# Kernel tuning notes

Hardware: AMD Instinct MI355X
Metric: run time of the kernel (lower is better)

## Reference

```python
import jax, jax.numpy as jnp
import numpy as np
from jax.ops import segment_sum

N_NODES = 100000


def _gcn_layer(x, W, b, src, dst, n_nodes):
    # DGL GraphConv with norm='both': out = D_in^{-1/2} A D_out^{-1/2} x W + b
    # degrees clamped to min 1 (DGL behavior, handles zero-degree nodes)
    ones_e = jnp.ones(src.shape[0], dtype=x.dtype)
    deg_out = jnp.clip(segment_sum(ones_e, src, num_segments=n_nodes), 1.0)
    deg_in = jnp.clip(segment_sum(ones_e, dst, num_segments=n_nodes), 1.0)
    h = x * jax.lax.rsqrt(deg_out)[:, None]            # [N, F] source norm
    agg = segment_sum(h[src], dst, num_segments=n_nodes)  # [N, F] sum over in-edges
    agg = agg * jax.lax.rsqrt(deg_in)[:, None]          # dest norm
    return agg @ W + b


def setup_inputs() -> dict:
    key = jax.random.key(0)
    k1, k2, k3, k4, k5 = jax.random.split(key, 5)
    E = 1600000
    x = jax.random.normal(k1, (N_NODES, 128), dtype=jnp.float32)
    edge_src = jax.random.randint(k2, (E,), 0, N_NODES, dtype=jnp.int32)
    edge_dst = jax.random.randint(k3, (E,), 0, N_NODES, dtype=jnp.int32)
    W1 = jax.random.normal(k4, (128, 64), dtype=jnp.float32) * (1.0 / np.sqrt(128))
    b1 = jnp.zeros((64,), dtype=jnp.float32)
    W2 = jax.random.normal(k5, (64, 64), dtype=jnp.float32) * (1.0 / np.sqrt(64))
    b2 = jnp.zeros((64,), dtype=jnp.float32)
    return {"x": x, "edge_src": edge_src, "edge_dst": edge_dst,
            "W1": W1, "b1": b1, "W2": W2, "b2": b2}


def reference(x, edge_src, edge_dst, W1, b1, W2, b2):
    h = _gcn_layer(x, W1, b1, edge_src, edge_dst, N_NODES)
    h = jax.nn.relu(h)
    out = _gcn_layer(h, W2, b2, edge_src, edge_dst, N_NODES)
    return out
```

## Files before the change

### kernel.cpp

```cpp
#include <hip/hip_runtime.h>
#include <hip/hip_fp16.h>


static inline size_t align256(size_t x) { return (x + 255) & ~(size_t)255; }

#define BKT_SHIFT 7
#define BKT_W 128
#define MAX_NBK 800
#define PA_BLOCKS 416

typedef _Float16 f16x8 __attribute__((ext_vector_type(8)));
typedef float f32x4 __attribute__((ext_vector_type(4)));

__global__ __launch_bounds__(256)
void part_hist_kernel(const int* __restrict__ src, const int* __restrict__ dst,
                      int* __restrict__ hist_d, int* __restrict__ hist_s,
                      int nbk, int E, int slice_len) {
    __shared__ int hd[MAX_NBK];
    __shared__ int hs[MAX_NBK];
    const int b = blockIdx.x;
    for (int i = threadIdx.x; i < nbk; i += 256) { hd[i] = 0; hs[i] = 0; }
    __syncthreads();
    const int beg = b * slice_len;
    const int end = min(beg + slice_len, E);
    for (int i = beg + threadIdx.x; i < end; i += 256) {
        atomicAdd(&hd[dst[i] >> BKT_SHIFT], 1);
        atomicAdd(&hs[src[i] >> BKT_SHIFT], 1);
    }
    __syncthreads();
    for (int i = threadIdx.x; i < nbk; i += 256) {
        hist_d[(size_t)i * PA_BLOCKS + b] = hd[i];
        hist_s[(size_t)i * PA_BLOCKS + b] = hs[i];
    }
}

__global__ __launch_bounds__(512)
void row_scan_kernel(int* __restrict__ hist_d, int* __restrict__ hist_s,
                     int* __restrict__ Td, int* __restrict__ Ts, int nbk) {
    __shared__ int tmp[512];
    int j = blockIdx.x;
    int* row;
    int* T;
    if (j < nbk) { row = hist_d + (size_t)j * PA_BLOCKS; T = Td; }
    else         { j -= nbk; row = hist_s + (size_t)j * PA_BLOCKS; T = Ts; }
    const int t = threadIdx.x;
    int v = (t < PA_BLOCKS) ? row[t] : 0;
    tmp[t] = v;
    __syncthreads();
    for (int off = 1; off < 512; off <<= 1) {
        int u = (t >= off) ? tmp[t - off] : 0;
        __syncthreads();
        tmp[t] += u;
        __syncthreads();
    }
    if (t < PA_BLOCKS) row[t] = tmp[t] - v;
    if (t == 511) T[j] = tmp[511];
}

__global__ __launch_bounds__(1024)
void tot_scan_kernel(int* __restrict__ Td, int* __restrict__ Ts, int nbk) {
    __shared__ int tmp[1024];
    const int t = threadIdx.x;
    int v = (t < nbk) ? Td[t] : 0;
    tmp[t] = v;
    __syncthreads();
    for (int off = 1; off < 1024; off <<= 1) {
        int u = (t >= off) ? tmp[t - off] : 0;
        __syncthreads();
        tmp[t] += u;
        __syncthreads();
    }
    if (t < nbk) Td[t] = tmp[t] - v;
    __syncthreads();
    int v2 = (t < nbk) ? Ts[t] : 0;
    tmp[t] = v2;
    __syncthreads();
    for (int off = 1; off < 1024; off <<= 1) {
        int u = (t >= off) ? tmp[t - off] : 0;
        __syncthreads();
        tmp[t] += u;
        __syncthreads();
    }
    if (t < nbk) Ts[t] = tmp[t] - v2;
}

__global__ __launch_bounds__(256)
void part_scatter_kernel(const int* __restrict__ src, const int* __restrict__ dst,
                         const int* __restrict__ hist_d, const int* __restrict__ hist_s,
                         const int* __restrict__ Td, const int* __restrict__ Ts,
                         int* __restrict__ ebuf, unsigned char* __restrict__ sbuf,
                         int nbk, int E, int slice_len) {
    __shared__ int cur_d[MAX_NBK];
    __shared__ int cur_s[MAX_NBK];
    const int b = blockIdx.x;
    for (int i = threadIdx.x; i < nbk; i += 256) {
        cur_d[i] = Td[i] + hist_d[(size_t)i * PA_BLOCKS + b];
        cur_s[i] = Ts[i] + hist_s[(size_t)i * PA_BLOCKS + b];
    }
    __syncthreads();
    const int beg = b * slice_len;
    const int end = min(beg + slice_len, E);
    for (int i = beg + threadIdx.x; i < end; i += 256) {
        int d = dst[i], s = src[i];
        int pd = atomicAdd(&cur_d[d >> BKT_SHIFT], 1);
        ebuf[pd] = ((d & (BKT_W - 1)) << 17) | s;
        int ps = atomicAdd(&cur_s[s >> BKT_SHIFT], 1);
        sbuf[ps] = (unsigned char)(s & (BKT_W - 1));
    }
}

__global__ __launch_bounds__(256)
void bucket_csr_kernel(const int* __restrict__ ebuf,
                       const unsigned char* __restrict__ sbuf,
                       const int* __restrict__ Td, const int* __restrict__ Ts,
                       int* __restrict__ csr_src,
                       int* __restrict__ cnt_in, int* __restrict__ cnt_out,
                       int* __restrict__ row_ptr,
                       int nbk, int N, int E) {
    __shared__ int cnt[BKT_W];
    __shared__ int rp[BKT_W];
    __shared__ int cur[BKT_W];
    __shared__ int cnts[BKT_W];
    const int k = blockIdx.x;
    const int lo = k << BKT_SHIFT;
    const int span = min(BKT_W, N - lo);
    const int db = Td[k], de = (k + 1 < nbk) ? Td[k + 1] : E;
    const int sb = Ts[k], se = (k + 1 < nbk) ? Ts[k + 1] : E;
    const int t = threadIdx.x;

    if (t < BKT_W) { cnt[t] = 0; cnts[t] = 0; }
    __syncthreads();
    for (int i = db + t; i < de; i += 256) atomicAdd(&cnt[ebuf[i] >> 17], 1);
    for (int i = sb + t; i < se; i += 256) atomicAdd(&cnts[sbuf[i]], 1);
    __syncthreads();
    if (t < BKT_W) rp[t] = cnt[t];
    __syncthreads();
    for (int off = 1; off < BKT_W; off <<= 1) {
        int v = (t < BKT_W && t >= off) ? rp[t - off] : 0;
        __syncthreads();
        if (t < BKT_W) rp[t] += v;
        __syncthreads();
    }
    if (t < span) {
        row_ptr[lo + t] = db + rp[t] - cnt[t];
        cnt_in[lo + t]  = cnt[t];
        cnt_out[lo + t] = cnts[t];
    }
    __syncthreads();
    if (t < BKT_W) cur[t] = db + rp[t] - cnt[t];
    __syncthreads();
    for (int i = db + t; i < de; i += 256) {
        int p = ebuf[i];
        int pos = atomicAdd(&cur[p >> 17], 1);
        csr_src[pos] = p & 0x1FFFF;
    }
    if (k == 0 && t == 0) row_ptr[N] = E;
}

template <int K>
__global__ __launch_bounds__(256)
void gemm_scale_kernel(const float* __restrict__ X, const float* __restrict__ W,
                       const int* __restrict__ cnt_out,
                       __half* __restrict__ Y, int N) {
    __shared__ _Float16 Wt[2][64][K + 8];
    const int t = threadIdx.x;
    for (int i = t; i < K * 64; i += 256) {
        const int k = i >> 6, j = i & 63;
        const float w = W[i];
        const _Float16 hi = (_Float16)w;
        Wt[0][j][k] = hi;
        Wt[1][j][k] = (_Float16)(w - (float)hi);
    }
    __syncthreads();

    const int wid  = t >> 6;
    const int lane = t & 63;
    const int col  = lane & 15;
    const int kg   = (lane >> 4) * 8;

    const int rowA = blockIdx.x * 64 + wid * 16 + col;
    const size_t xbase = (size_t)min(rowA, N - 1) * K;

    f32x4 acc0 = {}, acc1 = {}, acc2 = {}, acc3 = {};

#pragma unroll
    for (int ks = 0; ks < K; ks += 32) {
        float4 xa = *(const float4*)&X[xbase + ks + kg];
        float4 xb = *(const float4*)&X[xbase + ks + kg + 4];
        const float xs[8] = {xa.x, xa.y, xa.z, xa.w, xb.x, xb.y, xb.z, xb.w};
        f16x8 ahi, alo;
#pragma unroll
        for (int j = 0; j < 8; ++j) {
            const _Float16 h = (_Float16)xs[j];
            ahi[j] = h;
            alo[j] = (_Float16)(xs[j] - (float)h);
        }
#pragma unroll
        for (int tile = 0; tile < 4; ++tile) {
            const f16x8 bhi = *(const f16x8*)&Wt[0][col + 16 * tile][ks + kg];
            const f16x8 blo = *(const f16x8*)&Wt[1][col + 16 * tile][ks + kg];
            f32x4* acc = (tile == 0) ? &acc0 : (tile == 1) ? &acc1
                       : (tile == 2) ? &acc2 : &acc3;
            *acc = __builtin_amdgcn_mfma_f32_16x16x32_f16(ahi, bhi, *acc, 0, 0, 0);
            *acc = __builtin_amdgcn_mfma_f32_16x16x32_f16(alo, bhi, *acc, 0, 0, 0);
            *acc = __builtin_amdgcn_mfma_f32_16x16x32_f16(ahi, blo, *acc, 0, 0, 0);
        }
    }

    const int rbase = blockIdx.x * 64 + wid * 16 + (lane >> 4) * 4;
#pragma unroll
    for (int r = 0; r < 4; ++r) {
        const int rr = rbase + r;
        if (rr < N) {
            const float sc = rsqrtf((float)max(cnt_out[rr], 1));
            __half* yp = &Y[(size_t)rr * 64 + col];
            yp[0]  = __float2half_rn(acc0[r] * sc);
            yp[16] = __float2half_rn(acc1[r] * sc);
            yp[32] = __float2half_rn(acc2[r] * sc);
            yp[48] = __float2half_rn(acc3[r] * sc);
        }
    }
}

template <bool RELU>
__global__ __launch_bounds__(256)
void aggregate_kernel(const __half* __restrict__ Y,
                      const int* __restrict__ row_ptr,
                      const int* __restrict__ csr_src,
                      const int* __restrict__ cnt_in,
                      const float* __restrict__ bias,
                      float* __restrict__ out, int N) {
    const int n = blockIdx.x * 8 + (threadIdx.x >> 5);
    if (n >= N) return;
    const int fp = threadIdx.x & 31;

    const int start = row_ptr[n];
    const int end   = row_ptr[n + 1];
    const int last  = end - 1;

    float2 acc = {0.f, 0.f};
    for (int e = start; e < end; e += 16) {
        int idx[16];
#pragma unroll
        for (int j = 0; j < 16; ++j) idx[j] = csr_src[min(e + j, last)];
        float2 v[16];
#pragma unroll
        for (int j = 0; j < 16; ++j)
            v[j] = __half22float2(*((const __half2*)(Y + ((size_t)idx[j] << 6)) + fp));
#pragma unroll
        for (int j = 0; j < 16; ++j)
            if (e + j < end) { acc.x += v[j].x; acc.y += v[j].y; }
    }

    const float sc = rsqrtf((float)max(cnt_in[n], 1));
    float2 o;
    o.x = acc.x * sc + bias[2 * fp];
    o.y = acc.y * sc + bias[2 * fp + 1];
    if (RELU) { o.x = fmaxf(o.x, 0.f); o.y = fmaxf(o.y, 0.f); }
    *(float2*)&out[((size_t)n << 6) + 2 * fp] = o;
}

extern "C" void kernel_launch(void* const* d_in, const int* in_sizes, int n_in,
                              void* d_out, int out_size, void* d_ws, size_t ws_size,
                              hipStream_t stream) {
    const float* x   = (const float*)d_in[0];
    const int*   src = (const int*)d_in[1];
    const int*   dst = (const int*)d_in[2];
    const float* W1  = (const float*)d_in[3];
    const float* b1  = (const float*)d_in[4];
    const float* W2  = (const float*)d_in[5];
    const float* b2  = (const float*)d_in[6];
    float* out = (float*)d_out;

    const int N = in_sizes[0] / 128;
    const int E = in_sizes[1];

    const int nbk = (N + BKT_W - 1) >> BKT_SHIFT;
    const int M = nbk * PA_BLOCKS;

    char* ws = (char*)d_ws;
    size_t off = 0;
    __half* Y       = (__half*)(ws + off); off = align256(off + (size_t)N * 64 * sizeof(__half));
    int* csr_src    = (int*)(ws + off);    off = align256(off + (size_t)E * sizeof(int));
    int* ebuf       = (int*)(ws + off);    off = align256(off + (size_t)E * sizeof(int));
    unsigned char* sbuf = (unsigned char*)(ws + off); off = align256(off + (size_t)E);
    int* hist_d     = (int*)(ws + off);    off = align256(off + (size_t)M * sizeof(int));
    int* hist_s     = (int*)(ws + off);    off = align256(off + (size_t)M * sizeof(int));
    int* Td         = (int*)(ws + off);    off = align256(off + (size_t)nbk * sizeof(int));
    int* Ts         = (int*)(ws + off);    off = align256(off + (size_t)nbk * sizeof(int));
    int* cnt_out    = (int*)(ws + off);    off = align256(off + (size_t)N * sizeof(int));
    int* cnt_in     = (int*)(ws + off);    off = align256(off + (size_t)N * sizeof(int));
    int* row_ptr    = (int*)(ws + off);    off = align256(off + (size_t)(N + 1) * sizeof(int));

    const int pslice = (E + PA_BLOCKS - 1) / PA_BLOCKS;

    part_hist_kernel<<<PA_BLOCKS, 256, 0, stream>>>(src, dst, hist_d, hist_s, nbk, E, pslice);
    row_scan_kernel<<<2 * nbk, 512, 0, stream>>>(hist_d, hist_s, Td, Ts, nbk);
    tot_scan_kernel<<<1, 1024, 0, stream>>>(Td, Ts, nbk);
    part_scatter_kernel<<<PA_BLOCKS, 256, 0, stream>>>(src, dst, hist_d, hist_s, Td, Ts,
                                                       ebuf, sbuf, nbk, E, pslice);
    bucket_csr_kernel<<<nbk, 256, 0, stream>>>(ebuf, sbuf, Td, Ts, csr_src,
                                               cnt_in, cnt_out, row_ptr, nbk, N, E);

    const int gemm_blocks = (N + 63) / 64;
    const int agg_blocks  = (N + 7) / 8;

    gemm_scale_kernel<128><<<gemm_blocks, 256, 0, stream>>>(x, W1, cnt_out, Y, N);
    aggregate_kernel<true><<<agg_blocks, 256, 0, stream>>>(Y, row_ptr, csr_src, cnt_in, b1, out, N);

    gemm_scale_kernel<64><<<gemm_blocks, 256, 0, stream>>>(out, W2, cnt_out, Y, N);
    aggregate_kernel<false><<<agg_blocks, 256, 0, stream>>>(Y, row_ptr, csr_src, cnt_in, b2, out, N);
}
```

Before: 284.2 us.

## Fold bucket-total scan into scatter/CSR kernels and widen aggregate gathers

Removes the single-block tot_scan launch. part_scatter now computes exclusive prefixes of the bucket totals redundantly in each block, and bucket_csr derives its own bucket offsets with a block reduction over the preceding totals. The aggregate kernel now uses 16 lanes per node with 8-byte half4 loads, 12-edge batches and float4 stores, halving the threads per node. The goal is to cut a serialized launch and the per-edge load instruction count, at the cost of redundant scan work in every block.

```diff
diff --git a/kernel.cpp b/kernel.cpp
--- a/kernel.cpp
+++ b/kernel.cpp
@@ -57,33 +57,6 @@
     if (t == 511) T[j] = tmp[511];
 }
 
-__global__ __launch_bounds__(1024)
-void tot_scan_kernel(int* __restrict__ Td, int* __restrict__ Ts, int nbk) {
-    __shared__ int tmp[1024];
-    const int t = threadIdx.x;
-    int v = (t < nbk) ? Td[t] : 0;
-    tmp[t] = v;
-    __syncthreads();
-    for (int off = 1; off < 1024; off <<= 1) {
-        int u = (t >= off) ? tmp[t - off] : 0;
-        __syncthreads();
-        tmp[t] += u;
-        __syncthreads();
-    }
-    if (t < nbk) Td[t] = tmp[t] - v;
-    __syncthreads();
-    int v2 = (t < nbk) ? Ts[t] : 0;
-    tmp[t] = v2;
-    __syncthreads();
-    for (int off = 1; off < 1024; off <<= 1) {
-        int u = (t >= off) ? tmp[t - off] : 0;
-        __syncthreads();
-        tmp[t] += u;
-        __syncthreads();
-    }
-    if (t < nbk) Ts[t] = tmp[t] - v2;
-}
-
 __global__ __launch_bounds__(256)
 void part_scatter_kernel(const int* __restrict__ src, const int* __restrict__ dst,
                          const int* __restrict__ hist_d, const int* __restrict__ hist_s,
@@ -92,15 +65,48 @@
                          int nbk, int E, int slice_len) {
     __shared__ int cur_d[MAX_NBK];
     __shared__ int cur_s[MAX_NBK];
+    __shared__ int csum[256];
     const int b = blockIdx.x;
-    for (int i = threadIdx.x; i < nbk; i += 256) {
-        cur_d[i] = Td[i] + hist_d[(size_t)i * PA_BLOCKS + b];
-        cur_s[i] = Ts[i] + hist_s[(size_t)i * PA_BLOCKS + b];
-    }
-    __syncthreads();
+    const int t = threadIdx.x;
+
+#pragma unroll
+    for (int p = 0; p < 2; ++p) {
+        const int* T = p ? Ts : Td;
+        int* curx = p ? cur_s : cur_d;
+        const int base = 4 * t;
+        int v[4];
+        int s = 0;
+#pragma unroll
+        for (int q = 0; q < 4; ++q) {
+            v[q] = (base + q < nbk) ? T[base + q] : 0;
+            s += v[q];
+        }
+        csum[t] = s;
+        __syncthreads();
+        for (int off = 1; off < 256; off <<= 1) {
+            int u = (t >= off) ? csum[t - off] : 0;
+            __syncthreads();
+            csum[t] += u;
+            __syncthreads();
+        }
+        int run = csum[t] - s;
+#pragma unroll
+        for (int q = 0; q < 4; ++q) {
+            if (base + q < nbk) curx[base + q] = run;
+            run += v[q];
+        }
+        __syncthreads();
+    }
+
+    for (int i = t; i < nbk; i += 256) {
+        cur_d[i] += hist_d[(size_t)i * PA_BLOCKS + b];
+        cur_s[i] += hist_s[(size_t)i * PA_BLOCKS + b];
+    }
+    __syncthreads();
+
     const int beg = b * slice_len;
     const int end = min(beg + slice_len, E);
-    for (int i = beg + threadIdx.x; i < end; i += 256) {
+    for (int i = beg + t; i < end; i += 256) {
         int d = dst[i], s = src[i];
         int pd = atomicAdd(&cur_d[d >> BKT_SHIFT], 1);
         ebuf[pd] = ((d & (BKT_W - 1)) << 17) | s;
@@ -121,12 +127,33 @@
     __shared__ int rp[BKT_W];
     __shared__ int cur[BKT_W];
     __shared__ int cnts[BKT_W];
+    __shared__ int red[256];
+    __shared__ int sh_db, sh_sb;
     const int k = blockIdx.x;
     const int lo = k << BKT_SHIFT;
     const int span = min(BKT_W, N - lo);
-    const int db = Td[k], de = (k + 1 < nbk) ? Td[k + 1] : E;
-    const int sb = Ts[k], se = (k + 1 < nbk) ? Ts[k + 1] : E;
     const int t = threadIdx.x;
+
+    int s1 = 0, s2 = 0;
+    for (int i = t; i < k; i += 256) { s1 += Td[i]; s2 += Ts[i]; }
+    red[t] = s1;
+    __syncthreads();
+    for (int off = 128; off >= 1; off >>= 1) {
+        if (t < off) red[t] += red[t + off];
+        __syncthreads();
+    }
+    if (t == 0) sh_db = red[0];
+    __syncthreads();
+    red[t] = s2;
+    __syncthreads();
+    for (int off = 128; off >= 1; off >>= 1) {
+        if (t < off) red[t] += red[t + off];
+        __syncthreads();
+    }
+    if (t == 0) sh_sb = red[0];
+    __syncthreads();
+    const int db = sh_db, de = db + Td[k];
+    const int sb = sh_sb, se = sb + Ts[k];
 
     if (t < BKT_W) { cnt[t] = 0; cnts[t] = 0; }
     __syncthreads();
@@ -230,34 +257,45 @@
                       const int* __restrict__ cnt_in,
                       const float* __restrict__ bias,
                       float* __restrict__ out, int N) {
-    const int n = blockIdx.x * 8 + (threadIdx.x >> 5);
+    const int n = blockIdx.x * 16 + (threadIdx.x >> 4);
     if (n >= N) return;
-    const int fp = threadIdx.x & 31;
+    const int fq = threadIdx.x & 15;
 
     const int start = row_ptr[n];
     const int end   = row_ptr[n + 1];
     const int last  = end - 1;
 
-    float2 acc = {0.f, 0.f};
-    for (int e = start; e < end; e += 16) {
-        int idx[16];
-#pragma unroll
-        for (int j = 0; j < 16; ++j) idx[j] = csr_src[min(e + j, last)];
-        float2 v[16];
-#pragma unroll
-        for (int j = 0; j < 16; ++j)
-            v[j] = __half22float2(*((const __half2*)(Y + ((size_t)idx[j] << 6)) + fp));
-#pragma unroll
-        for (int j = 0; j < 16; ++j)
-            if (e + j < end) { acc.x += v[j].x; acc.y += v[j].y; }
+    float4 acc = {0.f, 0.f, 0.f, 0.f};
+    for (int e = start; e < end; e += 12) {
+        int idx[12];
+#pragma unroll
+        for (int j = 0; j < 12; ++j) idx[j] = csr_src[min(e + j, last)];
+        uint2 v[12];
+#pragma unroll
+        for (int j = 0; j < 12; ++j)
+            v[j] = *((const uint2*)(Y + ((size_t)idx[j] << 6)) + fq);
+#pragma unroll
+        for (int j = 0; j < 12; ++j) {
+            if (e + j < end) {
+                float2 a = __half22float2(*(const __half2*)&v[j].x);
+                float2 b = __half22float2(*(const __half2*)&v[j].y);
+                acc.x += a.x; acc.y += a.y; acc.z += b.x; acc.w += b.y;
+            }
+        }
     }
 
     const float sc = rsqrtf((float)max(cnt_in[n], 1));
-    float2 o;
-    o.x = acc.x * sc + bias[2 * fp];
-    o.y = acc.y * sc + bias[2 * fp + 1];
-    if (RELU) { o.x = fmaxf(o.x, 0.f); o.y = fmaxf(o.y, 0.f); }
-    *(float2*)&out[((size_t)n << 6) + 2 * fp] = o;
+    const float4 bb = *(const float4*)&bias[4 * fq];
+    float4 o;
+    o.x = acc.x * sc + bb.x;
+    o.y = acc.y * sc + bb.y;
+    o.z = acc.z * sc + bb.z;
+    o.w = acc.w * sc + bb.w;
+    if (RELU) {
+        o.x = fmaxf(o.x, 0.f); o.y = fmaxf(o.y, 0.f);
+        o.z = fmaxf(o.z, 0.f); o.w = fmaxf(o.w, 0.f);
+    }
+    *(float4*)&out[((size_t)n << 6) + 4 * fq] = o;
 }
 
 extern "C" void kernel_launch(void* const* d_in, const int* in_sizes, int n_in,
@@ -296,14 +334,13 @@
 
     part_hist_kernel<<<PA_BLOCKS, 256, 0, stream>>>(src, dst, hist_d, hist_s, nbk, E, pslice);
     row_scan_kernel<<<2 * nbk, 512, 0, stream>>>(hist_d, hist_s, Td, Ts, nbk);
-    tot_scan_kernel<<<1, 1024, 0, stream>>>(Td, Ts, nbk);
     part_scatter_kernel<<<PA_BLOCKS, 256, 0, stream>>>(src, dst, hist_d, hist_s, Td, Ts,
                                                        ebuf, sbuf, nbk, E, pslice);
     bucket_csr_kernel<<<nbk, 256, 0, stream>>>(ebuf, sbuf, Td, Ts, csr_src,
                                                cnt_in, cnt_out, row_ptr, nbk, N, E);
 
     const int gemm_blocks = (N + 63) / 64;
-    const int agg_blocks  = (N + 7) / 8;
+    const int agg_blocks  = (N + 15) / 16;
 
     gemm_scale_kernel<128><<<gemm_blocks, 256, 0, stream>>>(x, W1, cnt_out, Y, N);
     aggregate_kernel<true><<<agg_blocks, 256, 0, stream>>>(Y, row_ptr, csr_src, cnt_in, b1, out, N);
```

Result: faster. 267.4 us (-5.9%).
